# Optimization experiments

Measured on AMD Instinct MI355X. Metric: run time of the kernel, lower is better.

Reference implementation:

```python
import jax, jax.numpy as jnp
import numpy as np
import math

B, S, D, H = 4, 1024, 1024, 16
DK = D // H


def setup_inputs() -> dict:
    key = jax.random.key(0)
    ks = jax.random.split(key, 12)
    scale = 1.0 / math.sqrt(D)
    inp = {
        "query": jax.random.normal(ks[0], (B, S, D), jnp.float32),
        "key": jax.random.normal(ks[1], (B, S, D), jnp.float32),
        "value": jax.random.normal(ks[2], (B, S, D), jnp.float32),
        "mask": jnp.ones((B, S, S), jnp.int32),
        "Wq": jax.random.uniform(ks[3], (D, D), jnp.float32, -scale, scale),
        "bq": jax.random.uniform(ks[4], (D,), jnp.float32, -scale, scale),
        "Wk": jax.random.uniform(ks[5], (D, D), jnp.float32, -scale, scale),
        "bk": jax.random.uniform(ks[6], (D,), jnp.float32, -scale, scale),
        "Wv": jax.random.uniform(ks[7], (D, D), jnp.float32, -scale, scale),
        "bv": jax.random.uniform(ks[8], (D,), jnp.float32, -scale, scale),
        "Wo": jax.random.uniform(ks[9], (D, D), jnp.float32, -scale, scale),
        "bo": jax.random.uniform(ks[10], (D,), jnp.float32, -scale, scale),
    }
    return inp


def reference(query, key, value, mask, Wq, bq, Wk, bk, Wv, bv, Wo, bo):
    b, s, d = query.shape
    # QKV projections (torch Linear: x @ W.T + b), split into heads -> [b, h, s, dk]
    def proj(x, W, bias):
        return (x @ W.T + bias).reshape(b, -1, H, DK).transpose(0, 2, 1, 3)

    q = proj(query, Wq, bq)
    k = proj(key, Wk, bk)
    v = proj(value, Wv, bv)

    scores = jnp.einsum("bhqd,bhkd->bhqk", q, k) / jnp.sqrt(jnp.float32(DK))
    scores = jnp.where(mask[:, None, :, :] == 0, jnp.float32(-1e9), scores)
    p_attn = jax.nn.softmax(scores, axis=-1)  # dropout p=0.0 -> identity

    x = jnp.einsum("bhqk,bhkd->bhqd", p_attn, v)
    x = x.transpose(0, 2, 1, 3).reshape(b, -1, H * DK)  # [b, s, d]
    # F.threshold(x, 0.2, 0.0): values <= 0.2 replaced with 0
    x = jnp.where(x > 0.2, x, jnp.float32(0.0))
    x1 = x @ Wo.T + bo
    x1 = jnp.mean(x1, axis=-1, keepdims=True)
    return x + x1
```

## Files before the change

### kernel.cpp

```cpp
#include <hip/hip_runtime.h>
#include <hip/hip_bf16.h>
#include <math.h>

#define BB 4
#define SS 1024
#define DD 1024
#define NH 16
#define DKH 64

typedef __attribute__((ext_vector_type(8))) short bf16x8;
typedef __attribute__((ext_vector_type(4))) float f32x4;
typedef __attribute__((ext_vector_type(16))) float f32x16;

__device__ __forceinline__ ushort f2bf(float f) {
  __hip_bfloat16 h = __float2bfloat16(f);
  return *(ushort*)&h;
}

__device__ __forceinline__ bf16x8 pack8(float4 a, float4 b) {
  bf16x8 r;
  r[0] = (short)f2bf(a.x); r[1] = (short)f2bf(a.y);
  r[2] = (short)f2bf(a.z); r[3] = (short)f2bf(a.w);
  r[4] = (short)f2bf(b.x); r[5] = (short)f2bf(b.y);
  r[6] = (short)f2bf(b.z); r[7] = (short)f2bf(b.w);
  return r;
}

__device__ __forceinline__ void async16(const void* g, void* l) {
  __builtin_amdgcn_global_load_lds(
      (const __attribute__((address_space(1))) unsigned int*)g,
      (__attribute__((address_space(3))) unsigned int*)l, 16, 0, 0);
}

__global__ __launch_bounds__(256) void prep_all(
    const float* __restrict__ Xq, const float* __restrict__ Xk, const float* __restrict__ Xv,
    const int* __restrict__ mask,
    const float* __restrict__ Wq, const float* __restrict__ Wk, const float* __restrict__ Wv,
    const float* __restrict__ Wo, const float* __restrict__ bo,
    ushort* __restrict__ Wb, ushort* __restrict__ Ab,
    float* __restrict__ wo_sum, float* __restrict__ bo_mean,
    int* __restrict__ maskOK) {
  __shared__ int smi[4];
  const int bid = blockIdx.x;
  const int tid = threadIdx.x;

  if (bid < 64) {
    const int row0 = bid * 16;
    const int c = (tid + bid * 4) & 255;
    float4 acc = make_float4(0.f, 0.f, 0.f, 0.f);
#pragma unroll
    for (int r = 0; r < 16; ++r) {
      const float4 v = *(const float4*)(Wo + (size_t)(row0 + r) * DD + c * 4);
      acc.x += v.x; acc.y += v.y; acc.z += v.z; acc.w += v.w;
    }
    atomicAdd(&wo_sum[c * 4 + 0], acc.x);
    atomicAdd(&wo_sum[c * 4 + 1], acc.y);
    atomicAdd(&wo_sum[c * 4 + 2], acc.z);
    atomicAdd(&wo_sum[c * 4 + 3], acc.w);
    return;
  }

  if (bid == 64) {
    if (tid < 64) {
      float s = 0.f;
      for (int i = tid; i < 1024; i += 64) s += bo[i];
#pragma unroll
      for (int off = 1; off < 64; off <<= 1) s += __shfl_xor(s, off);
      if (tid == 0) *bo_mean = s * (1.0f / 1024.0f);
    }
    return;
  }

  if (bid < 577) {
    const int m = bid - 65;
    const int kt = m & 15, qt = (m >> 4) & 7, b = m >> 7;
    const int row = tid >> 1, half = tid & 1;
    const int* p = mask + ((size_t)b * SS + qt * 128 + row) * SS + kt * 64 + half * 32;
    int ok = 1;
#pragma unroll
    for (int j = 0; j < 8; ++j) {
      const int4 mm = *(const int4*)(p + j * 4);
      ok &= (mm.x != 0) & (mm.y != 0) & (mm.z != 0) & (mm.w != 0);
    }
    const unsigned long long bal = __ballot(ok);
    if ((tid & 63) == 0) smi[tid >> 6] = (bal == ~0ULL) ? 1 : 0;
    __syncthreads();
    if (tid == 0) maskOK[(b * 8 + qt) * 16 + kt] = smi[0] & smi[1] & smi[2] & smi[3];
    return;
  }

  if (bid < 1345) {
    const int c0 = bid - 577;
#pragma unroll
    for (int it = 0; it < 8; ++it) {
      const size_t g = (size_t)(c0 + it * 768) * 2048 + (size_t)tid * 8;
      const int t = (int)(g >> 22);
      const float* base = (t == 0) ? Xq : (t == 1) ? Xk : Xv;
      const size_t off = g & 4194303;
      const float4 f0 = *(const float4*)(base + off);
      const float4 f1 = *(const float4*)(base + off + 4);
      *(bf16x8*)(Ab + g) = pack8(f0, f1);
    }
    return;
  }

  {
    const int c0 = bid - 1345;
#pragma unroll
    for (int it = 0; it < 8; ++it) {
      const size_t g = (size_t)(c0 + it * 192) * 2048 + (size_t)tid * 8;
      const int t = (int)(g >> 20);
      const float* W = (t == 0) ? Wq : (t == 1) ? Wk : Wv;
      const size_t off = g & 1048575;
      const float4 f0 = *(const float4*)(W + off);
      const float4 f1 = *(const float4*)(W + off + 4);
      *(bf16x8*)(Wb + g) = pack8(f0, f1);
    }
  }
}

__global__ __launch_bounds__(256) void gemm_qkv_bf16(
    const ushort* __restrict__ Ab, const ushort* __restrict__ Wb,
    const float* __restrict__ bq, const float* __restrict__ bk, const float* __restrict__ bv,
    ushort* __restrict__ QKVb) {
  const int z = blockIdx.z;
  const char* A = (const char*)(Ab + (size_t)z * 4194304);
  const char* W = (const char*)(Wb + (size_t)z * 1048576);
  const float* bias = (z == 0) ? bq : (z == 1) ? bk : bv;
  ushort* Cz = QKVb + (size_t)z * 4194304;
  const float scale = (z == 0) ? 0.125f : 1.0f;

  __shared__ ushort As[8192];
  __shared__ ushort Ws[8192];

  const int tid = threadIdx.x;
  const int lane = tid & 63, w = tid >> 6;
  const int l31 = lane & 31, kh = lane >> 5;
  const int wn = w & 1, wm = w >> 1;
  const int m0 = blockIdx.x * 128, n0 = blockIdx.y * 128;

  const int r8 = lane >> 3;
  const int cg = (lane & 7) ^ r8;
  const int xr = l31 & 7;

  f32x16 acc[2][2];
#pragma unroll
  for (int mt = 0; mt < 2; ++mt)
#pragma unroll
    for (int nt = 0; nt < 2; ++nt)
#pragma unroll
      for (int r = 0; r < 16; ++r) acc[mt][nt][r] = 0.f;

  for (int k0 = 0; k0 < DD; k0 += 64) {
    __syncthreads();
#pragma unroll
    for (int t = 0; t < 4; ++t) {
      const int grp = w * 4 + t;
      const int row = grp * 8 + r8;
      async16(A + ((size_t)(m0 + row) * DD + k0 + cg * 8) * 2, &As[grp * 512]);
      async16(W + ((size_t)(n0 + row) * DD + k0 + cg * 8) * 2, &Ws[grp * 512]);
    }
    __syncthreads();
#pragma unroll
    for (int ks = 0; ks < 4; ++ks) {
      const int sc = (ks * 2 + kh) ^ xr;
      bf16x8 wf[2], af[2];
#pragma unroll
      for (int nt = 0; nt < 2; ++nt)
        wf[nt] = *(const bf16x8*)&Ws[(wn * 64 + nt * 32 + l31) * 64 + sc * 8];
#pragma unroll
      for (int mt = 0; mt < 2; ++mt)
        af[mt] = *(const bf16x8*)&As[(wm * 64 + mt * 32 + l31) * 64 + sc * 8];
#pragma unroll
      for (int mt = 0; mt < 2; ++mt)
#pragma unroll
        for (int nt = 0; nt < 2; ++nt)
          acc[mt][nt] = __builtin_amdgcn_mfma_f32_32x32x16_bf16(wf[nt], af[mt], acc[mt][nt], 0, 0, 0);
    }
  }

#pragma unroll
  for (int nt = 0; nt < 2; ++nt) {
#pragma unroll
    for (int g = 0; g < 4; ++g) {
      const int ng = n0 + wn * 64 + nt * 32 + kh * 4 + g * 8;
      const float4 b4 = *(const float4*)(bias + ng);
#pragma unroll
      for (int mt = 0; mt < 2; ++mt) {
        ushort4 pk;
        pk.x = f2bf((acc[mt][nt][g * 4 + 0] + b4.x) * scale);
        pk.y = f2bf((acc[mt][nt][g * 4 + 1] + b4.y) * scale);
        pk.z = f2bf((acc[mt][nt][g * 4 + 2] + b4.z) * scale);
        pk.w = f2bf((acc[mt][nt][g * 4 + 3] + b4.w) * scale);
        *(ushort4*)&Cz[(size_t)(m0 + wm * 64 + mt * 32 + l31) * DD + ng] = pk;
      }
    }
  }
}

__global__ __launch_bounds__(256) void flash_mfma(
    const ushort* __restrict__ QKVb, const int* __restrict__ mask,
    const int* __restrict__ maskOK, float* __restrict__ X) {
  __shared__ ushort Vt[64 * 72];
  __shared__ ushort Ps[128 * 72];

  const ushort* Qb = QKVb;
  const ushort* Kb = QKVb + 4194304;
  const ushort* Vb = QKVb + 8388608;

  const int tid = threadIdx.x;
  const int lane = tid & 63, w = tid >> 6;
  const int quad = lane >> 4, l15 = lane & 15;
  const int h = blockIdx.x, qblk = blockIdx.y, b = blockIdx.z;
  const int qbase = qblk * 128 + w * 32;

  bf16x8 qf[2][2];
#pragma unroll
  for (int qt = 0; qt < 2; ++qt)
#pragma unroll
    for (int ks = 0; ks < 2; ++ks)
      qf[qt][ks] = *(const bf16x8*)(Qb + (size_t)(b * SS + qbase + qt * 16 + l15) * DD +
                                    h * DKH + ks * 32 + quad * 8);

  unsigned okbits = 0;
  {
    const int* mkp = maskOK + (b * 8 + qblk) * 16;
#pragma unroll
    for (int i = 0; i < 16; ++i) okbits |= (mkp[i] ? 1u : 0u) << i;
  }

  f32x4 o[4][2];
  const f32x4 z4 = {0.f, 0.f, 0.f, 0.f};
#pragma unroll
  for (int dt = 0; dt < 4; ++dt)
#pragma unroll
    for (int qt = 0; qt < 2; ++qt) o[dt][qt] = z4;
  float l_run[2] = {0.f, 0.f};

  const int vp = tid & 31;
  const int vdc = tid >> 5;
  const ushort* Vg = Vb + (size_t)(b * SS) * DD + h * DKH + vdc * 8;
  const ushort* Kg = Kb + (size_t)(b * SS) * DD + h * DKH;
  uint* VtU = (uint*)Vt;
  const int* Mb = mask + (size_t)b * SS * SS;

  union U8 { uint4 u; ushort s[8]; };

  bf16x8 kf[4][2];
#pragma unroll
  for (int mt = 0; mt < 4; ++mt)
#pragma unroll
    for (int ks = 0; ks < 2; ++ks)
      kf[mt][ks] = *(const bf16x8*)(Kg + (size_t)(mt * 16 + l15) * DD + ks * 32 + quad * 8);
  U8 v0c, v1c;
  v0c.u = *(const uint4*)(Vg + (size_t)(2 * vp) * DD);
  v1c.u = *(const uint4*)(Vg + (size_t)(2 * vp + 1) * DD);

  for (int kt = 0; kt < 16; ++kt) {
    const int k064 = kt * 64;

    __builtin_amdgcn_s_barrier();
#pragma unroll
    for (int j = 0; j < 8; ++j)
      VtU[(vdc * 8 + j) * 36 + vp] = (uint)v0c.s[j] | ((uint)v1c.s[j] << 16);
    asm volatile("s_waitcnt lgkmcnt(0)" ::: "memory");
    __builtin_amdgcn_sched_barrier(0);
    __builtin_amdgcn_s_barrier();

    const int kn = (kt < 15) ? (k064 + 64) : 0;
    bf16x8 kfn[4][2];
#pragma unroll
    for (int mt = 0; mt < 4; ++mt)
#pragma unroll
      for (int ks = 0; ks < 2; ++ks)
        kfn[mt][ks] = *(const bf16x8*)(Kg + (size_t)(kn + mt * 16 + l15) * DD +
                                       ks * 32 + quad * 8);
    U8 v0n, v1n;
    v0n.u = *(const uint4*)(Vg + (size_t)(kn + 2 * vp) * DD);
    v1n.u = *(const uint4*)(Vg + (size_t)(kn + 2 * vp + 1) * DD);

    f32x4 s[4][2];
    __builtin_amdgcn_s_setprio(1);
#pragma unroll
    for (int mt = 0; mt < 4; ++mt)
#pragma unroll
      for (int qt = 0; qt < 2; ++qt) {
        f32x4 a = z4;
        a = __builtin_amdgcn_mfma_f32_16x16x32_bf16(kf[mt][0], qf[qt][0], a, 0, 0, 0);
        a = __builtin_amdgcn_mfma_f32_16x16x32_bf16(kf[mt][1], qf[qt][1], a, 0, 0, 0);
        s[mt][qt] = a;
      }
    __builtin_amdgcn_s_setprio(0);

    if (!((okbits >> kt) & 1)) {
#pragma unroll
      for (int mt = 0; mt < 4; ++mt)
#pragma unroll
        for (int qt = 0; qt < 2; ++qt)
#pragma unroll
          for (int reg = 0; reg < 4; ++reg) {
            const int q = qbase + qt * 16 + l15;
            const int key = k064 + mt * 16 + quad * 4 + reg;
            if (Mb[(size_t)q * SS + key] == 0) s[mt][qt][reg] = -1e9f;
          }
    }

#pragma unroll
    for (int qt = 0; qt < 2; ++qt) {
      float rs = 0.f;
#pragma unroll
      for (int mt = 0; mt < 4; ++mt) {
#pragma unroll
        for (int reg = 0; reg < 4; ++reg) {
          const float p = __expf(s[mt][qt][reg]);
          s[mt][qt][reg] = p;
          rs += p;
        }
      }
      l_run[qt] += rs;
#pragma unroll
      for (int mt = 0; mt < 4; ++mt) {
        ushort4 pk;
        pk.x = f2bf(s[mt][qt][0]);
        pk.y = f2bf(s[mt][qt][1]);
        pk.z = f2bf(s[mt][qt][2]);
        pk.w = f2bf(s[mt][qt][3]);
        *(ushort4*)&Ps[(w * 32 + qt * 16 + l15) * 72 + mt * 16 + quad * 4] = pk;
      }
    }

    bf16x8 pf[2][2];
#pragma unroll
    for (int qt = 0; qt < 2; ++qt)
#pragma unroll
      for (int ks = 0; ks < 2; ++ks)
        pf[qt][ks] = *(const bf16x8*)&Ps[(w * 32 + qt * 16 + l15) * 72 + ks * 32 + quad * 8];
    __builtin_amdgcn_s_setprio(1);
#pragma unroll
    for (int dt = 0; dt < 4; ++dt) {
      bf16x8 vf0 = *(const bf16x8*)&Vt[(dt * 16 + l15) * 72 + quad * 8];
      bf16x8 vf1 = *(const bf16x8*)&Vt[(dt * 16 + l15) * 72 + 32 + quad * 8];
#pragma unroll
      for (int qt = 0; qt < 2; ++qt) {
        o[dt][qt] = __builtin_amdgcn_mfma_f32_16x16x32_bf16(vf0, pf[qt][0], o[dt][qt], 0, 0, 0);
        o[dt][qt] = __builtin_amdgcn_mfma_f32_16x16x32_bf16(vf1, pf[qt][1], o[dt][qt], 0, 0, 0);
      }
    }
    __builtin_amdgcn_s_setprio(0);

#pragma unroll
    for (int mt = 0; mt < 4; ++mt)
#pragma unroll
      for (int ks = 0; ks < 2; ++ks)
        kf[mt][ks] = kfn[mt][ks];
    v0c.u = v0n.u;
    v1c.u = v1n.u;
  }

#pragma unroll
  for (int qt = 0; qt < 2; ++qt) {
    float l = l_run[qt];
    l += __shfl_xor(l, 16);
    l += __shfl_xor(l, 32);
    const float inv = 1.0f / l;
#pragma unroll
    for (int dt = 0; dt < 4; ++dt) {
      const f32x4 ov = o[dt][qt] * inv;
      *(f32x4*)(X + (size_t)(b * SS + qbase + qt * 16 + l15) * DD +
                h * DKH + dt * 16 + quad * 4) = ov;
    }
  }
}

__global__ __launch_bounds__(256) void epilogue_kernel(float* __restrict__ X,
                                                       const float* __restrict__ wo_sum,
                                                       const float* __restrict__ bo_mean) {
  __shared__ float red[4][4];
  const int tid = threadIdx.x;
  const float4 wv = *(const float4*)(wo_sum + tid * 4);
  const float bm = *bo_mean;
  float4 xt[4];
#pragma unroll
  for (int r = 0; r < 4; ++r) {
    const int row = blockIdx.x * 4 + r;
    const float4 x = *(const float4*)(X + (size_t)row * DD + tid * 4);
    xt[r].x = (x.x > 0.2f) ? x.x : 0.f;
    xt[r].y = (x.y > 0.2f) ? x.y : 0.f;
    xt[r].z = (x.z > 0.2f) ? x.z : 0.f;
    xt[r].w = (x.w > 0.2f) ? x.w : 0.f;
    float part = xt[r].x * wv.x + xt[r].y * wv.y + xt[r].z * wv.z + xt[r].w * wv.w;
#pragma unroll
    for (int off = 1; off < 64; off <<= 1) part += __shfl_xor(part, off);
    if ((tid & 63) == 0) red[r][tid >> 6] = part;
  }
  __syncthreads();
#pragma unroll
  for (int r = 0; r < 4; ++r) {
    const int row = blockIdx.x * 4 + r;
    const float x1 = ((red[r][0] + red[r][1]) + (red[r][2] + red[r][3])) * (1.0f / 1024.0f) + bm;
    const float4 o = make_float4(xt[r].x + x1, xt[r].y + x1, xt[r].z + x1, xt[r].w + x1);
    *(float4*)(X + (size_t)row * DD + tid * 4) = o;
  }
}

extern "C" void kernel_launch(void* const* d_in, const int* in_sizes, int n_in,
                              void* d_out, int out_size, void* d_ws, size_t ws_size,
                              hipStream_t stream) {
  const float* Xq = (const float*)d_in[0];
  const float* Xk = (const float*)d_in[1];
  const float* Xv = (const float*)d_in[2];
  const int* mask = (const int*)d_in[3];
  const float* Wq = (const float*)d_in[4];
  const float* bq = (const float*)d_in[5];
  const float* Wk = (const float*)d_in[6];
  const float* bk = (const float*)d_in[7];
  const float* Wv = (const float*)d_in[8];
  const float* bv = (const float*)d_in[9];
  const float* Wo = (const float*)d_in[10];
  const float* bo = (const float*)d_in[11];

  ushort* Wb = (ushort*)d_ws;
  ushort* Ab = Wb + (size_t)3 * 1048576;
  ushort* QKVb = Ab + (size_t)3 * 4194304;
  float* wo_sum = (float*)(QKVb + (size_t)3 * 4194304);
  float* bo_mean = wo_sum + 1024;
  int* maskOK = (int*)(bo_mean + 1);
  float* X = (float*)d_out;

  hipMemsetAsync(wo_sum, 0, 1024 * sizeof(float), stream);

  prep_all<<<1537, 256, 0, stream>>>(Xq, Xk, Xv, mask, Wq, Wk, Wv, Wo, bo,
                                     Wb, Ab, wo_sum, bo_mean, maskOK);

  gemm_qkv_bf16<<<dim3(32, 8, 3), 256, 0, stream>>>(Ab, Wb, bq, bk, bv, QKVb);

  flash_mfma<<<dim3(16, 8, 4), 256, 0, stream>>>(QKVb, mask, maskOK, X);

  epilogue_kernel<<<1024, 256, 0, stream>>>(X, wo_sum, bo_mean);
}
```

Measured before the change: 216.4 us.

## Split attention key range in two and merge partial sums in epilogue

The flash attention kernel now splits each head's 1024 keys into two halves handled by separate blocks, doubling the grid. Each half writes its unnormalized output and row sums to separate buffers, one of which reuses the bf16 activation workspace. The epilogue combines the two partials and normalizes before the threshold and the mean projection. This is meant to raise occupancy and parallelism in the attention stage, at the cost of an extra full-size fp32 write and read plus the per-row sum buffers.

```diff
diff --git a/kernel.cpp b/kernel.cpp
--- a/kernel.cpp
+++ b/kernel.cpp
@@ -200,7 +200,9 @@
 
 __global__ __launch_bounds__(256) void flash_mfma(
     const ushort* __restrict__ QKVb, const int* __restrict__ mask,
-    const int* __restrict__ maskOK, float* __restrict__ X) {
+    const int* __restrict__ maskOK, float* __restrict__ X0,
+    float* __restrict__ X1, float* __restrict__ l0buf,
+    float* __restrict__ l1buf) {
   __shared__ ushort Vt[64 * 72];
   __shared__ ushort Ps[128 * 72];
 
@@ -211,8 +213,11 @@
   const int tid = threadIdx.x;
   const int lane = tid & 63, w = tid >> 6;
   const int quad = lane >> 4, l15 = lane & 15;
-  const int h = blockIdx.x, qblk = blockIdx.y, b = blockIdx.z;
+  const int hx = blockIdx.x;
+  const int h = hx >> 1, khalf = hx & 1;
+  const int qblk = blockIdx.y, b = blockIdx.z;
   const int qbase = qblk * 128 + w * 32;
+  const int kbase = khalf * 512;
 
   bf16x8 qf[2][2];
 #pragma unroll
@@ -251,13 +256,14 @@
   for (int mt = 0; mt < 4; ++mt)
 #pragma unroll
     for (int ks = 0; ks < 2; ++ks)
-      kf[mt][ks] = *(const bf16x8*)(Kg + (size_t)(mt * 16 + l15) * DD + ks * 32 + quad * 8);
+      kf[mt][ks] = *(const bf16x8*)(Kg + (size_t)(kbase + mt * 16 + l15) * DD +
+                                    ks * 32 + quad * 8);
   U8 v0c, v1c;
-  v0c.u = *(const uint4*)(Vg + (size_t)(2 * vp) * DD);
-  v1c.u = *(const uint4*)(Vg + (size_t)(2 * vp + 1) * DD);
-
-  for (int kt = 0; kt < 16; ++kt) {
-    const int k064 = kt * 64;
+  v0c.u = *(const uint4*)(Vg + (size_t)(kbase + 2 * vp) * DD);
+  v1c.u = *(const uint4*)(Vg + (size_t)(kbase + 2 * vp + 1) * DD);
+
+  for (int kt = 0; kt < 8; ++kt) {
+    const int k064 = kbase + kt * 64;
 
     __builtin_amdgcn_s_barrier();
 #pragma unroll
@@ -267,7 +273,7 @@
     __builtin_amdgcn_sched_barrier(0);
     __builtin_amdgcn_s_barrier();
 
-    const int kn = (kt < 15) ? (k064 + 64) : 0;
+    const int kn = (kt < 7) ? (k064 + 64) : kbase;
     bf16x8 kfn[4][2];
 #pragma unroll
     for (int mt = 0; mt < 4; ++mt)
@@ -292,7 +298,7 @@
       }
     __builtin_amdgcn_s_setprio(0);
 
-    if (!((okbits >> kt) & 1)) {
+    if (!((okbits >> (khalf * 8 + kt)) & 1)) {
 #pragma unroll
       for (int mt = 0; mt < 4; ++mt)
 #pragma unroll
@@ -357,33 +363,43 @@
     v1c.u = v1n.u;
   }
 
+  float* Xout = khalf ? X1 : X0;
+  float* lout = khalf ? l1buf : l0buf;
 #pragma unroll
   for (int qt = 0; qt < 2; ++qt) {
     float l = l_run[qt];
     l += __shfl_xor(l, 16);
     l += __shfl_xor(l, 32);
-    const float inv = 1.0f / l;
+    const int row = b * SS + qbase + qt * 16 + l15;
+    if (quad == 0) lout[(size_t)row * NH + h] = l;
 #pragma unroll
     for (int dt = 0; dt < 4; ++dt) {
-      const f32x4 ov = o[dt][qt] * inv;
-      *(f32x4*)(X + (size_t)(b * SS + qbase + qt * 16 + l15) * DD +
-                h * DKH + dt * 16 + quad * 4) = ov;
-    }
-  }
-}
-
-__global__ __launch_bounds__(256) void epilogue_kernel(float* __restrict__ X,
-                                                       const float* __restrict__ wo_sum,
-                                                       const float* __restrict__ bo_mean) {
+      *(f32x4*)(Xout + (size_t)row * DD + h * DKH + dt * 16 + quad * 4) = o[dt][qt];
+    }
+  }
+}
+
+__global__ __launch_bounds__(256) void epilogue_kernel(
+    float* __restrict__ X, const float* __restrict__ X0,
+    const float* __restrict__ l0buf, const float* __restrict__ l1buf,
+    const float* __restrict__ wo_sum, const float* __restrict__ bo_mean) {
   __shared__ float red[4][4];
   const int tid = threadIdx.x;
   const float4 wv = *(const float4*)(wo_sum + tid * 4);
   const float bm = *bo_mean;
+  const int hh = tid >> 4;
   float4 xt[4];
 #pragma unroll
   for (int r = 0; r < 4; ++r) {
     const int row = blockIdx.x * 4 + r;
-    const float4 x = *(const float4*)(X + (size_t)row * DD + tid * 4);
+    const float4 a = *(const float4*)(X0 + (size_t)row * DD + tid * 4);
+    const float4 c = *(const float4*)(X + (size_t)row * DD + tid * 4);
+    const float inv = 1.0f / (l0buf[(size_t)row * NH + hh] + l1buf[(size_t)row * NH + hh]);
+    float4 x;
+    x.x = (a.x + c.x) * inv;
+    x.y = (a.y + c.y) * inv;
+    x.z = (a.z + c.z) * inv;
+    x.w = (a.w + c.w) * inv;
     xt[r].x = (x.x > 0.2f) ? x.x : 0.f;
     xt[r].y = (x.y > 0.2f) ? x.y : 0.f;
     xt[r].z = (x.z > 0.2f) ? x.z : 0.f;
@@ -425,6 +441,9 @@
   float* wo_sum = (float*)(QKVb + (size_t)3 * 4194304);
   float* bo_mean = wo_sum + 1024;
   int* maskOK = (int*)(bo_mean + 1);
+  float* X0 = (float*)Ab;
+  float* l0buf = X0 + (size_t)4096 * 1024;
+  float* l1buf = l0buf + 65536;
   float* X = (float*)d_out;
 
   hipMemsetAsync(wo_sum, 0, 1024 * sizeof(float), stream);
@@ -434,7 +453,8 @@
 
   gemm_qkv_bf16<<<dim3(32, 8, 3), 256, 0, stream>>>(Ab, Wb, bq, bk, bv, QKVb);
 
-  flash_mfma<<<dim3(16, 8, 4), 256, 0, stream>>>(QKVb, mask, maskOK, X);
-
-  epilogue_kernel<<<1024, 256, 0, stream>>>(X, wo_sum, bo_mean);
-}
+  flash_mfma<<<dim3(32, 8, 4), 256, 0, stream>>>(QKVb, mask, maskOK, X0, X,
+                                                 l0buf, l1buf);
+
+  epilogue_kernel<<<1024, 256, 0, stream>>>(X, X0, l0buf, l1buf, wo_sum, bo_mean);
+}
```

Result: slower. 233.4 us (+7.9%).

## Store QKV head-major and stage K tiles in LDS via async double-buffered loads

Applied to the files above, without the earlier changes.

The projection epilogue now writes Q/K/V in a head-major [head][batch*seq][64] layout, so each attention block reads contiguous 128-byte rows instead of rows strided by the full model width. K tiles are no longer loaded redundantly into registers by every wave. Instead they are fetched once per block with async global-to-LDS copies into a swizzled, double-buffered shared buffer and read from LDS for the QK^T MFMAs. This cuts redundant global traffic and register pressure, but adds LDS use and relies on the async copies being complete by the existing wait and barrier.

```diff
diff --git a/kernel.cpp b/kernel.cpp
--- a/kernel.cpp
+++ b/kernel.cpp
@@ -179,20 +179,23 @@
     }
   }
 
+  const int hh = blockIdx.y * 2 + wn;
 #pragma unroll
   for (int nt = 0; nt < 2; ++nt) {
 #pragma unroll
     for (int g = 0; g < 4; ++g) {
       const int ng = n0 + wn * 64 + nt * 32 + kh * 4 + g * 8;
+      const int d = nt * 32 + kh * 4 + g * 8;
       const float4 b4 = *(const float4*)(bias + ng);
 #pragma unroll
       for (int mt = 0; mt < 2; ++mt) {
+        const int row = m0 + wm * 64 + mt * 32 + l31;
         ushort4 pk;
         pk.x = f2bf((acc[mt][nt][g * 4 + 0] + b4.x) * scale);
         pk.y = f2bf((acc[mt][nt][g * 4 + 1] + b4.y) * scale);
         pk.z = f2bf((acc[mt][nt][g * 4 + 2] + b4.z) * scale);
         pk.w = f2bf((acc[mt][nt][g * 4 + 3] + b4.w) * scale);
-        *(ushort4*)&Cz[(size_t)(m0 + wm * 64 + mt * 32 + l31) * DD + ng] = pk;
+        *(ushort4*)&Cz[(size_t)hh * 262144 + (size_t)row * 64 + d] = pk;
       }
     }
   }
@@ -201,12 +204,9 @@
 __global__ __launch_bounds__(256) void flash_mfma(
     const ushort* __restrict__ QKVb, const int* __restrict__ mask,
     const int* __restrict__ maskOK, float* __restrict__ X) {
+  __shared__ ushort Ks[2][4096];
   __shared__ ushort Vt[64 * 72];
   __shared__ ushort Ps[128 * 72];
-
-  const ushort* Qb = QKVb;
-  const ushort* Kb = QKVb + 4194304;
-  const ushort* Vb = QKVb + 8388608;
 
   const int tid = threadIdx.x;
   const int lane = tid & 63, w = tid >> 6;
@@ -214,13 +214,17 @@
   const int h = blockIdx.x, qblk = blockIdx.y, b = blockIdx.z;
   const int qbase = qblk * 128 + w * 32;
 
+  const ushort* Qh = QKVb + (size_t)h * 262144;
+  const ushort* Kh = QKVb + 4194304 + (size_t)h * 262144 + (size_t)(b * SS) * 64;
+  const ushort* Vh = QKVb + 8388608 + (size_t)h * 262144 + (size_t)(b * SS) * 64;
+
   bf16x8 qf[2][2];
 #pragma unroll
   for (int qt = 0; qt < 2; ++qt)
 #pragma unroll
     for (int ks = 0; ks < 2; ++ks)
-      qf[qt][ks] = *(const bf16x8*)(Qb + (size_t)(b * SS + qbase + qt * 16 + l15) * DD +
-                                    h * DKH + ks * 32 + quad * 8);
+      qf[qt][ks] = *(const bf16x8*)(Qh + (size_t)(b * SS + qbase + qt * 16 + l15) * 64 +
+                                    ks * 32 + quad * 8);
 
   unsigned okbits = 0;
   {
@@ -239,57 +243,59 @@
 
   const int vp = tid & 31;
   const int vdc = tid >> 5;
-  const ushort* Vg = Vb + (size_t)(b * SS) * DD + h * DKH + vdc * 8;
-  const ushort* Kg = Kb + (size_t)(b * SS) * DD + h * DKH;
+  const ushort* Vg = Vh + vdc * 8;
   uint* VtU = (uint*)Vt;
   const int* Mb = mask + (size_t)b * SS * SS;
 
+  const int r8k = tid >> 3;
+  const int gk = (tid & 7) ^ (r8k & 7);
+  const int xk = l15 & 7;
+
   union U8 { uint4 u; ushort s[8]; };
 
-  bf16x8 kf[4][2];
-#pragma unroll
-  for (int mt = 0; mt < 4; ++mt)
-#pragma unroll
-    for (int ks = 0; ks < 2; ++ks)
-      kf[mt][ks] = *(const bf16x8*)(Kg + (size_t)(mt * 16 + l15) * DD + ks * 32 + quad * 8);
+  async16(Kh + (size_t)r8k * 64 + gk * 8, &Ks[0][(size_t)tid * 8]);
+  async16(Kh + (size_t)(32 + r8k) * 64 + gk * 8, &Ks[0][2048 + (size_t)tid * 8]);
   U8 v0c, v1c;
-  v0c.u = *(const uint4*)(Vg + (size_t)(2 * vp) * DD);
-  v1c.u = *(const uint4*)(Vg + (size_t)(2 * vp + 1) * DD);
+  v0c.u = *(const uint4*)(Vg + (size_t)(2 * vp) * 64);
+  v1c.u = *(const uint4*)(Vg + (size_t)(2 * vp + 1) * 64);
 
   for (int kt = 0; kt < 16; ++kt) {
     const int k064 = kt * 64;
+    const int cur = kt & 1;
 
     __builtin_amdgcn_s_barrier();
 #pragma unroll
     for (int j = 0; j < 8; ++j)
       VtU[(vdc * 8 + j) * 36 + vp] = (uint)v0c.s[j] | ((uint)v1c.s[j] << 16);
+    if (kt < 15) {
+      const ushort* Kt = Kh + (size_t)(k064 + 64) * 64;
+      async16(Kt + (size_t)r8k * 64 + gk * 8, &Ks[cur ^ 1][(size_t)tid * 8]);
+      async16(Kt + (size_t)(32 + r8k) * 64 + gk * 8, &Ks[cur ^ 1][2048 + (size_t)tid * 8]);
+    }
     asm volatile("s_waitcnt lgkmcnt(0)" ::: "memory");
     __builtin_amdgcn_sched_barrier(0);
     __builtin_amdgcn_s_barrier();
 
     const int kn = (kt < 15) ? (k064 + 64) : 0;
-    bf16x8 kfn[4][2];
-#pragma unroll
-    for (int mt = 0; mt < 4; ++mt)
-#pragma unroll
-      for (int ks = 0; ks < 2; ++ks)
-        kfn[mt][ks] = *(const bf16x8*)(Kg + (size_t)(kn + mt * 16 + l15) * DD +
-                                       ks * 32 + quad * 8);
     U8 v0n, v1n;
-    v0n.u = *(const uint4*)(Vg + (size_t)(kn + 2 * vp) * DD);
-    v1n.u = *(const uint4*)(Vg + (size_t)(kn + 2 * vp + 1) * DD);
+    v0n.u = *(const uint4*)(Vg + (size_t)(kn + 2 * vp) * 64);
+    v1n.u = *(const uint4*)(Vg + (size_t)(kn + 2 * vp + 1) * 64);
 
     f32x4 s[4][2];
     __builtin_amdgcn_s_setprio(1);
 #pragma unroll
-    for (int mt = 0; mt < 4; ++mt)
+    for (int mt = 0; mt < 4; ++mt) {
+      const int rr = mt * 16 + l15;
+      bf16x8 kf0 = *(const bf16x8*)&Ks[cur][rr * 64 + ((quad) ^ xk) * 8];
+      bf16x8 kf1 = *(const bf16x8*)&Ks[cur][rr * 64 + ((4 + quad) ^ xk) * 8];
 #pragma unroll
       for (int qt = 0; qt < 2; ++qt) {
         f32x4 a = z4;
-        a = __builtin_amdgcn_mfma_f32_16x16x32_bf16(kf[mt][0], qf[qt][0], a, 0, 0, 0);
-        a = __builtin_amdgcn_mfma_f32_16x16x32_bf16(kf[mt][1], qf[qt][1], a, 0, 0, 0);
+        a = __builtin_amdgcn_mfma_f32_16x16x32_bf16(kf0, qf[qt][0], a, 0, 0, 0);
+        a = __builtin_amdgcn_mfma_f32_16x16x32_bf16(kf1, qf[qt][1], a, 0, 0, 0);
         s[mt][qt] = a;
       }
+    }
     __builtin_amdgcn_s_setprio(0);
 
     if (!((okbits >> kt) & 1)) {
@@ -348,11 +354,6 @@
     }
     __builtin_amdgcn_s_setprio(0);
 
-#pragma unroll
-    for (int mt = 0; mt < 4; ++mt)
-#pragma unroll
-      for (int ks = 0; ks < 2; ++ks)
-        kf[mt][ks] = kfn[mt][ks];
     v0c.u = v0n.u;
     v1c.u = v1n.u;
   }
```

Result: no change. 214.8 us (-0.7%).
